# Performance work log

Measured on AMD Instinct MI355X. Metric: run time of the kernel, lower is better.

Reference implementation:

```python
import jax, jax.numpy as jnp
import numpy as np

D_MODEL = 512
NUM_HEADS = 8
HEAD_DIM = D_MODEL // NUM_HEADS
LN_EPS = 1e-5


def setup_inputs() -> dict:
    key = jax.random.key(0)
    ks = jax.random.split(key, 12)
    B, S, D = 4, 8192, D_MODEL
    scale = 1.0 / np.sqrt(D)  # xavier-ish init
    inp = {
        "x": jax.random.normal(ks[0], (B, S, D), dtype=jnp.float32),
        "Wq": jax.random.normal(ks[1], (D, D), dtype=jnp.float32) * scale,
        "bq": jnp.zeros((D,), dtype=jnp.float32),
        "Wk": jax.random.normal(ks[2], (D, D), dtype=jnp.float32) * scale,
        "bk": jnp.zeros((D,), dtype=jnp.float32),
        "Wv": jax.random.normal(ks[3], (D, D), dtype=jnp.float32) * scale,
        "bv": jnp.zeros((D,), dtype=jnp.float32),
        "Wo": jax.random.normal(ks[4], (D, D), dtype=jnp.float32) * scale,
        "bo": jnp.zeros((D,), dtype=jnp.float32),
        "gamma": jnp.ones((D,), dtype=jnp.float32),
        "beta": jnp.zeros((D,), dtype=jnp.float32),
    }
    return inp


def _split_heads(t, B, S):
    # (B, S, D) -> (B, H, S, hd)
    return t.reshape(B, S, NUM_HEADS, HEAD_DIM).transpose(0, 2, 1, 3)


def _feature_map(t):
    return jax.nn.elu(t) + 1.0


def reference(x, Wq, bq, Wk, bk, Wv, bv, Wo, bo, gamma, beta):
    B, S, D = x.shape
    q = _split_heads(x @ Wq + bq, B, S)
    k = _split_heads(x @ Wk + bk, B, S)
    v = _split_heads(x @ Wv + bv, B, S)

    q = _feature_map(q)
    k = _feature_map(k)

    # kv summary: (B, H, hd, hd) -- O(n d^2) instead of O(n^2 d)
    kv = jnp.einsum('bhnd,bhnm->bhdm', k, v)
    out = jnp.einsum('bhnd,bhdm->bhnm', q, kv)

    k_sum = k.sum(axis=2)  # (B, H, hd)
    normalizer = jnp.clip(jnp.einsum('bhnd,bhd->bhn', q, k_sum), 1e-6, None)
    out = out / normalizer[..., None]

    # merge heads: (B, H, S, hd) -> (B, S, D)
    out = out.transpose(0, 2, 1, 3).reshape(B, S, D)
    out = out @ Wo + bo

    # residual + layer norm (dropout is identity in eval / p=0)
    y = x + out
    mean = y.mean(axis=-1, keepdims=True)
    var = y.var(axis=-1, keepdims=True)
    y = (y - mean) * jax.lax.rsqrt(var + LN_EPS)
    return y * gamma + beta
```

## Files before the change

kernel.cpp:

```cpp
#include <hip/hip_runtime.h>
#include <cstdint>

#define SEQ     8192
#define BATCH   4
#define NHEAD   8
#define NTOK    (BATCH*SEQ)

typedef __bf16 bf16x8 __attribute__((ext_vector_type(8)));
typedef float  floatx4 __attribute__((ext_vector_type(4)));

static __device__ __forceinline__ float b2f(uint16_t h) {
    return __uint_as_float(((uint32_t)h) << 16);
}
static __device__ __forceinline__ uint16_t f2b(float f) {
    uint32_t u = __float_as_uint(f);
    u += 0x7fffu + ((u >> 16) & 1u);
    return (uint16_t)(u >> 16);
}

static __device__ __forceinline__ void async_copy16(const uint16_t* g, uint16_t* l) {
#if __has_builtin(__builtin_amdgcn_global_load_lds)
    __builtin_amdgcn_global_load_lds(
        (const __attribute__((address_space(1))) void*)g,
        (__attribute__((address_space(3))) void*)l, 16, 0, 0);
#else
    *(uint4*)l = *(const uint4*)g;
#endif
}

__global__ __launch_bounds__(256) void convert_x(
    const float* __restrict__ X, uint16_t* __restrict__ Xb)
{
    const size_t i = ((size_t)blockIdx.x * 256 + threadIdx.x) * 8;
    float4 f0 = *(const float4*)(X + i);
    float4 f1 = *(const float4*)(X + i + 4);
    uint4 o;
    uint16_t* p = (uint16_t*)&o;
    p[0]=f2b(f0.x); p[1]=f2b(f0.y); p[2]=f2b(f0.z); p[3]=f2b(f0.w);
    p[4]=f2b(f1.x); p[5]=f2b(f1.y); p[6]=f2b(f1.z); p[7]=f2b(f1.w);
    *(uint4*)(Xb + i) = o;
}

__global__ __launch_bounds__(256) void convert_w(
    const float* __restrict__ Wq, const float* __restrict__ Wk,
    const float* __restrict__ Wv, const float* __restrict__ Wo,
    uint16_t* __restrict__ out)
{
    const int z = blockIdx.z;
    const float* W = (z == 0) ? Wq : (z == 1) ? Wk : (z == 2) ? Wv : Wo;
    uint16_t* o = out + (size_t)z * 262144;
    const int n0 = blockIdx.x * 64, k0 = blockIdx.y * 64;
    __shared__ uint16_t tl[64][64];
    const int t = threadIdx.x;
    const int r  = t >> 4;
    const int c4 = (t & 15) * 4;
    #pragma unroll
    for (int s = 0; s < 4; ++s) {
        const int k = r + s * 16;
        float4 f = *(const float4*)(W + (size_t)(k0 + k) * 512 + n0 + c4);
        tl[c4 + 0][k] = f2b(f.x); tl[c4 + 1][k] = f2b(f.y);
        tl[c4 + 2][k] = f2b(f.z); tl[c4 + 3][k] = f2b(f.w);
    }
    __syncthreads();
    const int n  = t >> 2;
    const int kk = (t & 3) * 16;
    uint4* dst = (uint4*)(o + (size_t)(n0 + n) * 512 + k0 + kk);
    dst[0] = *(const uint4*)&tl[n][kk];
    dst[1] = *(const uint4*)&tl[n][kk + 8];
}

__global__ __launch_bounds__(256) void qkv128(
    const uint16_t* __restrict__ Xb,
    const uint16_t* __restrict__ Wt,
    const float* __restrict__ bq_, const float* __restrict__ bk_,
    const float* __restrict__ bv_,
    uint16_t* __restrict__ outQ, uint16_t* __restrict__ outK,
    uint16_t* __restrict__ outV)
{
    const int id = blockIdx.x;
    const int c  = id & 7;
    const int r_ = id >> 3;
    const int j_ = r_ % 12;
    const int s  = (r_ / 12) * 8 + c;
    const int proj = j_ >> 2;
    const int n0   = (j_ & 3) * 128;
    const int m0   = s * 128;

    const uint16_t* W = Wt + (size_t)proj * 262144;
    const float* bias = (proj == 0) ? bq_ : (proj == 1) ? bk_ : bv_;
    uint16_t* out     = (proj == 0) ? outQ : (proj == 1) ? outK : outV;
    const int act = (proj < 2);

    __shared__ uint16_t smem[8192];
    const int t = threadIdx.x;
    const int wave = t >> 6, lane = t & 63, quad = lane >> 4, lrow = lane & 15;
    const int wm = (wave & 1) * 64, wn = (wave >> 1) * 64;
    const int sr = t >> 2;
    const int sc = (t & 3) * 8;

    floatx4 acc[4][4] = {};

    for (int k0 = 0; k0 < 512; k0 += 32) {
        const uint16_t* gA = Xb + (size_t)(m0 + sr) * 512 + k0 + sc;
        async_copy16(gA,            smem + t * 8);
        async_copy16(gA + 64 * 512, smem + (t + 256) * 8);
        const uint16_t* gB = W + (size_t)(n0 + sr) * 512 + k0 + sc;
        async_copy16(gB,            smem + 4096 + t * 8);
        async_copy16(gB + 64 * 512, smem + 4096 + (t + 256) * 8);
        __syncthreads();
        bf16x8 af[4], bfr[4];
        #pragma unroll
        for (int i = 0; i < 4; ++i)
            af[i] = *(const bf16x8*)(smem + (wm + i * 16 + lrow) * 32 + quad * 8);
        #pragma unroll
        for (int j = 0; j < 4; ++j)
            bfr[j] = *(const bf16x8*)(smem + 4096 + (wn + j * 16 + lrow) * 32 + quad * 8);
        #pragma unroll
        for (int i = 0; i < 4; ++i)
            #pragma unroll
            for (int j = 0; j < 4; ++j)
                acc[i][j] = __builtin_amdgcn_mfma_f32_16x16x32_bf16(af[i], bfr[j], acc[i][j], 0, 0, 0);
        __syncthreads();
    }

    #pragma unroll
    for (int hh = 0; hh < 2; ++hh) {
        if ((wave & 1) == hh) {
            #pragma unroll
            for (int j = 0; j < 4; ++j) {
                const int col = wn + j * 16 + lrow;
                const float bb = bias[n0 + col];
                #pragma unroll
                for (int i = 0; i < 4; ++i) {
                    #pragma unroll
                    for (int r = 0; r < 4; ++r) {
                        const int lr = i * 16 + quad * 4 + r;
                        float v = acc[i][j][r] + bb;
                        if (act) v = (v > 0.0f) ? (v + 1.0f) : __expf(v);
                        smem[lr * 128 + (col ^ (((lr >> 2) & 3) << 4))] = f2b(v);
                    }
                }
            }
        }
        __syncthreads();
        #pragma unroll
        for (int p = 0; p < 4; ++p) {
            const int idx = p * 256 + t;
            const int row = idx >> 4;
            const int cc  = (idx & 15) * 8;
            uint4 v = *(const uint4*)(smem + row * 128 + (cc ^ (((row >> 2) & 3) << 4)));
            *(uint4*)(out + (size_t)(m0 + hh * 64 + row) * 512 + n0 + cc) = v;
        }
        __syncthreads();
    }
}

__global__ __launch_bounds__(256) void gemm_out128(
    const uint16_t* __restrict__ A,
    const uint16_t* __restrict__ Wt,
    const float* __restrict__ bias,
    const float* __restrict__ resid,
    uint16_t* __restrict__ out)
{
    const int id = blockIdx.x;
    const int c  = id & 7;
    const int r_ = id >> 3;
    const int j_ = r_ & 3;
    const int s  = (r_ >> 2) * 8 + c;
    const int n0 = j_ * 128;
    const int m0 = s * 128;

    __shared__ uint16_t smem[8192];
    const int t = threadIdx.x;
    const int wave = t >> 6, lane = t & 63, quad = lane >> 4, lrow = lane & 15;
    const int wm = (wave & 1) * 64, wn = (wave >> 1) * 64;
    const int sr = t >> 2;
    const int sc = (t & 3) * 8;

    floatx4 acc[4][4] = {};

    for (int k0 = 0; k0 < 512; k0 += 32) {
        const uint16_t* gA = A + (size_t)(m0 + sr) * 512 + k0 + sc;
        async_copy16(gA,            smem + t * 8);
        async_copy16(gA + 64 * 512, smem + (t + 256) * 8);
        const uint16_t* gB = Wt + (size_t)(n0 + sr) * 512 + k0 + sc;
        async_copy16(gB,            smem + 4096 + t * 8);
        async_copy16(gB + 64 * 512, smem + 4096 + (t + 256) * 8);
        __syncthreads();
        bf16x8 af[4], bfr[4];
        #pragma unroll
        for (int i = 0; i < 4; ++i)
            af[i] = *(const bf16x8*)(smem + (wm + i * 16 + lrow) * 32 + quad * 8);
        #pragma unroll
        for (int j = 0; j < 4; ++j)
            bfr[j] = *(const bf16x8*)(smem + 4096 + (wn + j * 16 + lrow) * 32 + quad * 8);
        #pragma unroll
        for (int i = 0; i < 4; ++i)
            #pragma unroll
            for (int j = 0; j < 4; ++j)
                acc[i][j] = __builtin_amdgcn_mfma_f32_16x16x32_bf16(af[i], bfr[j], acc[i][j], 0, 0, 0);
        __syncthreads();
    }

    #pragma unroll
    for (int hh = 0; hh < 2; ++hh) {
        if ((wave & 1) == hh) {
            #pragma unroll
            for (int j = 0; j < 4; ++j) {
                const int col = wn + j * 16 + lrow;
                const float bb = bias[n0 + col];
                #pragma unroll
                for (int i = 0; i < 4; ++i) {
                    #pragma unroll
                    for (int r = 0; r < 4; ++r) {
                        const int lr = i * 16 + quad * 4 + r;
                        float v = acc[i][j][r] + bb
                                + resid[(size_t)(m0 + hh * 64 + lr) * 512 + n0 + col];
                        smem[lr * 128 + (col ^ (((lr >> 2) & 3) << 4))] = f2b(v);
                    }
                }
            }
        }
        __syncthreads();
        #pragma unroll
        for (int p = 0; p < 4; ++p) {
            const int idx = p * 256 + t;
            const int row = idx >> 4;
            const int cc  = (idx & 15) * 8;
            uint4 v = *(const uint4*)(smem + row * 128 + (cc ^ (((row >> 2) & 3) << 4)));
            *(uint4*)(out + (size_t)(m0 + hh * 64 + row) * 512 + n0 + cc) = v;
        }
        __syncthreads();
    }
}

__global__ __launch_bounds__(256) void kv_accum(
    const uint16_t* __restrict__ K,
    const uint16_t* __restrict__ V,
    float* __restrict__ KV,
    float* __restrict__ KSUM)
{
    const int chunk = blockIdx.x;
    const int h     = blockIdx.y;
    const int b     = blockIdx.z;
    const int t    = threadIdx.x;
    const int wv   = t >> 6;
    const int lane = t & 63;
    const int quad = lane >> 4;
    const int lrow = lane & 15;

    __shared__ uint16_t kt[64 * 72];
    __shared__ uint16_t vt[64 * 72];

    floatx4 acc[4] = {};
    floatx4 accS = {};
    union { uint16_t u[8]; bf16x8 v; } one_u;
    #pragma unroll
    for (int j = 0; j < 8; ++j) one_u.u[j] = 0x3F80;
    const bf16x8 ones = one_u.v;

    const size_t base = ((size_t)(b * SEQ + chunk * 512)) * 512 + h * 64;

    for (int n0 = 0; n0 < 512; n0 += 64) {
        #pragma unroll
        for (int s = 0; s < 2; ++s) {
            const int i   = t + 256 * s;
            const int tok = i >> 3;
            const int d0  = (i & 7) * 8;
            uint4 kq = *(const uint4*)(K + base + (size_t)(n0 + tok) * 512 + d0);
            const uint16_t* kp = (const uint16_t*)&kq;
            #pragma unroll
            for (int j = 0; j < 8; ++j) kt[(d0 + j) * 72 + tok] = kp[j];
            uint4 vq = *(const uint4*)(V + base + (size_t)(n0 + tok) * 512 + d0);
            const uint16_t* vp = (const uint16_t*)&vq;
            #pragma unroll
            for (int j = 0; j < 8; ++j) vt[(d0 + j) * 72 + tok] = vp[j];
        }
        __syncthreads();
        #pragma unroll
        for (int ks = 0; ks < 2; ++ks) {
            bf16x8 af = *(const bf16x8*)(kt + (wv * 16 + lrow) * 72 + ks * 32 + quad * 8);
            accS = __builtin_amdgcn_mfma_f32_16x16x32_bf16(af, ones, accS, 0, 0, 0);
            #pragma unroll
            for (int nt = 0; nt < 4; ++nt) {
                bf16x8 bf = *(const bf16x8*)(vt + (nt * 16 + lrow) * 72 + ks * 32 + quad * 8);
                acc[nt] = __builtin_amdgcn_mfma_f32_16x16x32_bf16(af, bf, acc[nt], 0, 0, 0);
            }
        }
        __syncthreads();
    }

    float* kvp = KV + (size_t)(b * NHEAD + h) * 4096;
    #pragma unroll
    for (int nt = 0; nt < 4; ++nt) {
        const int m = nt * 16 + lrow;
        #pragma unroll
        for (int r = 0; r < 4; ++r) {
            const int d = wv * 16 + quad * 4 + r;
            atomicAdd(kvp + d * 64 + m, acc[nt][r]);
        }
    }
    if (lrow == 0) {
        float* kp = KSUM + (size_t)(b * NHEAD + h) * 64;
        #pragma unroll
        for (int r = 0; r < 4; ++r)
            atomicAdd(kp + wv * 16 + quad * 4 + r, accS[r]);
    }
}

__global__ __launch_bounds__(256) void attn_apply(
    const uint16_t* __restrict__ Q,
    const float* __restrict__ KVg,
    const float* __restrict__ KSg,
    uint16_t* __restrict__ OUT)
{
    const int h    = blockIdx.y;
    const int tok0 = blockIdx.x * 64;
    const int b    = tok0 >> 13;
    const int t    = threadIdx.x;
    const int wv   = t >> 6;
    const int lane = t & 63;
    const int quad = lane >> 4;
    const int lrow = lane & 15;

    __shared__ uint16_t bt[64 * 72];
    __shared__ uint16_t ksb[64];

    const float* kvp = KVg + (size_t)(b * NHEAD + h) * 4096;
    #pragma unroll
    for (int s = 0; s < 16; ++s) {
        const int e = t + 256 * s;
        const int d = e >> 6, m = e & 63;
        bt[m * 72 + d] = f2b(kvp[e]);
    }
    if (t < 64) ksb[t] = f2b(KSg[(size_t)(b * NHEAD + h) * 64 + t]);
    __syncthreads();

    floatx4 acc[4] = {};
    floatx4 accN = {};
    const uint16_t* qrow = Q + (size_t)(tok0 + wv * 16 + lrow) * 512 + h * 64 + quad * 8;
    #pragma unroll
    for (int ks = 0; ks < 2; ++ks) {
        bf16x8 af = *(const bf16x8*)(qrow + ks * 32);
        bf16x8 bks = *(const bf16x8*)(ksb + ks * 32 + quad * 8);
        accN = __builtin_amdgcn_mfma_f32_16x16x32_bf16(af, bks, accN, 0, 0, 0);
        #pragma unroll
        for (int nt = 0; nt < 4; ++nt) {
            bf16x8 bf = *(const bf16x8*)(bt + (nt * 16 + lrow) * 72 + ks * 32 + quad * 8);
            acc[nt] = __builtin_amdgcn_mfma_f32_16x16x32_bf16(af, bf, acc[nt], 0, 0, 0);
        }
    }

    __syncthreads();
    #pragma unroll
    for (int r = 0; r < 4; ++r) {
        const float inv = 1.0f / fmaxf(accN[r], 1e-6f);
        const int row = wv * 16 + quad * 4 + r;
        #pragma unroll
        for (int nt = 0; nt < 4; ++nt) {
            const int col = nt * 16 + lrow;
            bt[row * 64 + (col ^ (((row >> 2) & 3) << 4))] = f2b(acc[nt][r] * inv);
        }
    }
    __syncthreads();
    #pragma unroll
    for (int p = 0; p < 2; ++p) {
        const int idx = p * 256 + t;
        const int row = idx >> 3;
        const int cc  = (idx & 7) * 8;
        uint4 v = *(const uint4*)(bt + row * 64 + (cc ^ (((row >> 2) & 3) << 4)));
        *(uint4*)(OUT + (size_t)(tok0 + row) * 512 + h * 64 + cc) = v;
    }
}

__global__ __launch_bounds__(256) void ln_rows(
    const uint16_t* __restrict__ Z,
    const float* __restrict__ gamma,
    const float* __restrict__ beta,
    float* __restrict__ OUT)
{
    const int t = threadIdx.x;
    const int wv = t >> 6, lane = t & 63;
    const size_t row = (size_t)blockIdx.x * 4 + wv;
    union { uint4 q; uint16_t u[8]; } zz;
    zz.q = *(const uint4*)(Z + row * 512 + lane * 8);
    float v[8], s = 0.f, s2 = 0.f;
    #pragma unroll
    for (int j = 0; j < 8; ++j) {
        v[j] = b2f(zz.u[j]);
        s += v[j]; s2 += v[j] * v[j];
    }
    #pragma unroll
    for (int off = 32; off > 0; off >>= 1) {
        s  += __shfl_xor(s, off, 64);
        s2 += __shfl_xor(s2, off, 64);
    }
    const float mean = s * (1.0f / 512.0f);
    const float var  = s2 * (1.0f / 512.0f) - mean * mean;
    const float inv  = rsqrtf(var + 1e-5f);
    float4 g0 = *(const float4*)(gamma + lane * 8);
    float4 g1 = *(const float4*)(gamma + lane * 8 + 4);
    float4 b0 = *(const float4*)(beta + lane * 8);
    float4 b1 = *(const float4*)(beta + lane * 8 + 4);
    float4 o0, o1;
    o0.x = (v[0]-mean)*inv*g0.x + b0.x;  o0.y = (v[1]-mean)*inv*g0.y + b0.y;
    o0.z = (v[2]-mean)*inv*g0.z + b0.z;  o0.w = (v[3]-mean)*inv*g0.w + b0.w;
    o1.x = (v[4]-mean)*inv*g1.x + b1.x;  o1.y = (v[5]-mean)*inv*g1.y + b1.y;
    o1.z = (v[6]-mean)*inv*g1.z + b1.z;  o1.w = (v[7]-mean)*inv*g1.w + b1.w;
    *(float4*)(OUT + row * 512 + lane * 8)     = o0;
    *(float4*)(OUT + row * 512 + lane * 8 + 4) = o1;
}

extern "C" void kernel_launch(void* const* d_in, const int* in_sizes, int n_in,
                              void* d_out, int out_size, void* d_ws, size_t ws_size,
                              hipStream_t stream)
{
    (void)in_sizes; (void)n_in; (void)out_size; (void)ws_size;
    const float* x     = (const float*)d_in[0];
    const float* Wq    = (const float*)d_in[1];
    const float* bq    = (const float*)d_in[2];
    const float* Wk    = (const float*)d_in[3];
    const float* bk    = (const float*)d_in[4];
    const float* Wv    = (const float*)d_in[5];
    const float* bv    = (const float*)d_in[6];
    const float* Wo    = (const float*)d_in[7];
    const float* bo    = (const float*)d_in[8];
    const float* gamma = (const float*)d_in[9];
    const float* beta  = (const float*)d_in[10];

    uint8_t* ws = (uint8_t*)d_ws;
    float*    KV   = (float*)ws;
    float*    KSUM = (float*)(ws + (size_t)32 * 4096 * 4);
    uint16_t* Wt   = (uint16_t*)(ws + (size_t)32 * 4096 * 4 + 32 * 64 * 4);
    uint16_t* phiQ = (uint16_t*)(ws + (size_t)32 * 4096 * 4 + 32 * 64 * 4
                                    + (size_t)4 * 262144 * 2);
    uint16_t* Xb   = phiQ + (size_t)NTOK * 512;
    uint16_t* phiK = (uint16_t*)d_out;
    uint16_t* vbuf = (uint16_t*)d_out + (size_t)NTOK * 512;
    uint16_t* attn = Xb;
    uint16_t* zbuf = phiQ;

    hipMemsetAsync(ws, 0, (size_t)32 * 4096 * 4 + 32 * 64 * 4, stream);

    dim3 blk(256);
    convert_x<<<dim3(NTOK * 512 / (256 * 8)), blk, 0, stream>>>(x, Xb);
    convert_w<<<dim3(8, 8, 4), blk, 0, stream>>>(Wq, Wk, Wv, Wo, Wt);
    qkv128<<<dim3(3072), blk, 0, stream>>>(
        Xb, Wt, bq, bk, bv, phiQ, phiK, vbuf);
    kv_accum<<<dim3(16, NHEAD, BATCH), blk, 0, stream>>>(phiK, vbuf, KV, KSUM);
    attn_apply<<<dim3(NTOK / 64, NHEAD), blk, 0, stream>>>(phiQ, KV, KSUM, attn);
    gemm_out128<<<dim3(1024), blk, 0, stream>>>(
        attn, Wt + (size_t)3 * 262144, bo, x, zbuf);
    ln_rows<<<dim3(NTOK / 4), blk, 0, stream>>>(zbuf, gamma, beta, (float*)d_out);
}
```

Measured before the change: 306.5 us.

## Double-buffer GEMM k-loop, single-pass epilogue, and shrink LDS padding

The QKV and output-projection GEMMs now double-buffer their LDS tiles. The next k-slice's async global-to-LDS copies are issued before the MFMAs on the current slice, so that load latency can overlap compute and one barrier per iteration is removed. The epilogues now stage the full 128x128 tile in the doubled LDS and store it in one pass instead of two halves. The kv_accum and attn_apply kernels change their LDS row padding from 72 to 66 elements to reduce LDS footprint and bank conflicts. The 66-element stride breaks 16-byte alignment for the bf16x8 vector LDS reads, which risks misaligned or split accesses. The doubled GEMM LDS allocation may also lower occupancy.

```diff
diff --git a/kernel.cpp b/kernel.cpp
--- a/kernel.cpp
+++ b/kernel.cpp
@@ -91,67 +91,75 @@
     uint16_t* out     = (proj == 0) ? outQ : (proj == 1) ? outK : outV;
     const int act = (proj < 2);
 
-    __shared__ uint16_t smem[8192];
+    __shared__ uint16_t smem[16384];
     const int t = threadIdx.x;
     const int wave = t >> 6, lane = t & 63, quad = lane >> 4, lrow = lane & 15;
     const int wm = (wave & 1) * 64, wn = (wave >> 1) * 64;
     const int sr = t >> 2;
     const int sc = (t & 3) * 8;
 
+    const uint16_t* gA = Xb + (size_t)(m0 + sr) * 512 + sc;
+    const uint16_t* gB = W  + (size_t)(n0 + sr) * 512 + sc;
+
     floatx4 acc[4][4] = {};
 
+    async_copy16(gA,            smem + t * 8);
+    async_copy16(gA + 64 * 512, smem + (t + 256) * 8);
+    async_copy16(gB,            smem + 4096 + t * 8);
+    async_copy16(gB + 64 * 512, smem + 4096 + (t + 256) * 8);
+    __syncthreads();
+
+    int cur = 0;
     for (int k0 = 0; k0 < 512; k0 += 32) {
-        const uint16_t* gA = Xb + (size_t)(m0 + sr) * 512 + k0 + sc;
-        async_copy16(gA,            smem + t * 8);
-        async_copy16(gA + 64 * 512, smem + (t + 256) * 8);
-        const uint16_t* gB = W + (size_t)(n0 + sr) * 512 + k0 + sc;
-        async_copy16(gB,            smem + 4096 + t * 8);
-        async_copy16(gB + 64 * 512, smem + 4096 + (t + 256) * 8);
-        __syncthreads();
+        const int nxt = cur ^ 1;
+        if (k0 + 32 < 512) {
+            const uint16_t* pA = gA + k0 + 32;
+            async_copy16(pA,            smem + nxt * 8192 + t * 8);
+            async_copy16(pA + 64 * 512, smem + nxt * 8192 + (t + 256) * 8);
+            const uint16_t* pB = gB + k0 + 32;
+            async_copy16(pB,            smem + nxt * 8192 + 4096 + t * 8);
+            async_copy16(pB + 64 * 512, smem + nxt * 8192 + 4096 + (t + 256) * 8);
+        }
+        const uint16_t* base = smem + cur * 8192;
         bf16x8 af[4], bfr[4];
         #pragma unroll
         for (int i = 0; i < 4; ++i)
-            af[i] = *(const bf16x8*)(smem + (wm + i * 16 + lrow) * 32 + quad * 8);
+            af[i] = *(const bf16x8*)(base + (wm + i * 16 + lrow) * 32 + quad * 8);
         #pragma unroll
         for (int j = 0; j < 4; ++j)
-            bfr[j] = *(const bf16x8*)(smem + 4096 + (wn + j * 16 + lrow) * 32 + quad * 8);
+            bfr[j] = *(const bf16x8*)(base + 4096 + (wn + j * 16 + lrow) * 32 + quad * 8);
         #pragma unroll
         for (int i = 0; i < 4; ++i)
             #pragma unroll
             for (int j = 0; j < 4; ++j)
                 acc[i][j] = __builtin_amdgcn_mfma_f32_16x16x32_bf16(af[i], bfr[j], acc[i][j], 0, 0, 0);
         __syncthreads();
-    }
-
-    #pragma unroll
-    for (int hh = 0; hh < 2; ++hh) {
-        if ((wave & 1) == hh) {
-            #pragma unroll
-            for (int j = 0; j < 4; ++j) {
-                const int col = wn + j * 16 + lrow;
-                const float bb = bias[n0 + col];
-                #pragma unroll
-                for (int i = 0; i < 4; ++i) {
-                    #pragma unroll
-                    for (int r = 0; r < 4; ++r) {
-                        const int lr = i * 16 + quad * 4 + r;
-                        float v = acc[i][j][r] + bb;
-                        if (act) v = (v > 0.0f) ? (v + 1.0f) : __expf(v);
-                        smem[lr * 128 + (col ^ (((lr >> 2) & 3) << 4))] = f2b(v);
-                    }
-                }
+        cur = nxt;
+    }
+
+    #pragma unroll
+    for (int j = 0; j < 4; ++j) {
+        const int col = wn + j * 16 + lrow;
+        const float bb = bias[n0 + col];
+        #pragma unroll
+        for (int i = 0; i < 4; ++i) {
+            #pragma unroll
+            for (int r = 0; r < 4; ++r) {
+                const int row = wm + i * 16 + quad * 4 + r;
+                float v = acc[i][j][r] + bb;
+                if (act) v = (v > 0.0f) ? (v + 1.0f) : __expf(v);
+                smem[row * 128 + (col ^ (((row >> 2) & 3) << 4))] = f2b(v);
             }
         }
-        __syncthreads();
-        #pragma unroll
-        for (int p = 0; p < 4; ++p) {
-            const int idx = p * 256 + t;
-            const int row = idx >> 4;
-            const int cc  = (idx & 15) * 8;
-            uint4 v = *(const uint4*)(smem + row * 128 + (cc ^ (((row >> 2) & 3) << 4)));
-            *(uint4*)(out + (size_t)(m0 + hh * 64 + row) * 512 + n0 + cc) = v;
-        }
-        __syncthreads();
+    }
+    __syncthreads();
+    #pragma unroll
+    for (int p = 0; p < 8; ++p) {
+        const int idx = p * 256 + t;
+        const int row = idx >> 4;
+        const int cc  = (idx & 15) * 8;
+        uint4 v = *(const uint4*)(smem + row * 128 + (cc ^ (((row >> 2) & 3) << 4)));
+        *(uint4*)(out + (size_t)(m0 + row) * 512 + n0 + cc) = v;
     }
 }
 
@@ -170,67 +178,75 @@
     const int n0 = j_ * 128;
     const int m0 = s * 128;
 
-    __shared__ uint16_t smem[8192];
+    __shared__ uint16_t smem[16384];
     const int t = threadIdx.x;
     const int wave = t >> 6, lane = t & 63, quad = lane >> 4, lrow = lane & 15;
     const int wm = (wave & 1) * 64, wn = (wave >> 1) * 64;
     const int sr = t >> 2;
     const int sc = (t & 3) * 8;
 
+    const uint16_t* gA = A  + (size_t)(m0 + sr) * 512 + sc;
+    const uint16_t* gB = Wt + (size_t)(n0 + sr) * 512 + sc;
+
     floatx4 acc[4][4] = {};
 
+    async_copy16(gA,            smem + t * 8);
+    async_copy16(gA + 64 * 512, smem + (t + 256) * 8);
+    async_copy16(gB,            smem + 4096 + t * 8);
+    async_copy16(gB + 64 * 512, smem + 4096 + (t + 256) * 8);
+    __syncthreads();
+
+    int cur = 0;
     for (int k0 = 0; k0 < 512; k0 += 32) {
-        const uint16_t* gA = A + (size_t)(m0 + sr) * 512 + k0 + sc;
-        async_copy16(gA,            smem + t * 8);
-        async_copy16(gA + 64 * 512, smem + (t + 256) * 8);
-        const uint16_t* gB = Wt + (size_t)(n0 + sr) * 512 + k0 + sc;
-        async_copy16(gB,            smem + 4096 + t * 8);
-        async_copy16(gB + 64 * 512, smem + 4096 + (t + 256) * 8);
-        __syncthreads();
+        const int nxt = cur ^ 1;
+        if (k0 + 32 < 512) {
+            const uint16_t* pA = gA + k0 + 32;
+            async_copy16(pA,            smem + nxt * 8192 + t * 8);
+            async_copy16(pA + 64 * 512, smem + nxt * 8192 + (t + 256) * 8);
+            const uint16_t* pB = gB + k0 + 32;
+            async_copy16(pB,            smem + nxt * 8192 + 4096 + t * 8);
+            async_copy16(pB + 64 * 512, smem + nxt * 8192 + 4096 + (t + 256) * 8);
+        }
+        const uint16_t* base = smem + cur * 8192;
         bf16x8 af[4], bfr[4];
         #pragma unroll
         for (int i = 0; i < 4; ++i)
-            af[i] = *(const bf16x8*)(smem + (wm + i * 16 + lrow) * 32 + quad * 8);
+            af[i] = *(const bf16x8*)(base + (wm + i * 16 + lrow) * 32 + quad * 8);
         #pragma unroll
         for (int j = 0; j < 4; ++j)
-            bfr[j] = *(const bf16x8*)(smem + 4096 + (wn + j * 16 + lrow) * 32 + quad * 8);
+            bfr[j] = *(const bf16x8*)(base + 4096 + (wn + j * 16 + lrow) * 32 + quad * 8);
         #pragma unroll
         for (int i = 0; i < 4; ++i)
             #pragma unroll
             for (int j = 0; j < 4; ++j)
                 acc[i][j] = __builtin_amdgcn_mfma_f32_16x16x32_bf16(af[i], bfr[j], acc[i][j], 0, 0, 0);
         __syncthreads();
-    }
-
-    #pragma unroll
-    for (int hh = 0; hh < 2; ++hh) {
-        if ((wave & 1) == hh) {
-            #pragma unroll
-            for (int j = 0; j < 4; ++j) {
-                const int col = wn + j * 16 + lrow;
-                const float bb = bias[n0 + col];
-                #pragma unroll
-                for (int i = 0; i < 4; ++i) {
-                    #pragma unroll
-                    for (int r = 0; r < 4; ++r) {
-                        const int lr = i * 16 + quad * 4 + r;
-                        float v = acc[i][j][r] + bb
-                                + resid[(size_t)(m0 + hh * 64 + lr) * 512 + n0 + col];
-                        smem[lr * 128 + (col ^ (((lr >> 2) & 3) << 4))] = f2b(v);
-                    }
-                }
+        cur = nxt;
+    }
+
+    #pragma unroll
+    for (int j = 0; j < 4; ++j) {
+        const int col = wn + j * 16 + lrow;
+        const float bb = bias[n0 + col];
+        #pragma unroll
+        for (int i = 0; i < 4; ++i) {
+            #pragma unroll
+            for (int r = 0; r < 4; ++r) {
+                const int row = wm + i * 16 + quad * 4 + r;
+                float v = acc[i][j][r] + bb
+                        + resid[(size_t)(m0 + row) * 512 + n0 + col];
+                smem[row * 128 + (col ^ (((row >> 2) & 3) << 4))] = f2b(v);
             }
         }
-        __syncthreads();
-        #pragma unroll
-        for (int p = 0; p < 4; ++p) {
-            const int idx = p * 256 + t;
-            const int row = idx >> 4;
-            const int cc  = (idx & 15) * 8;
-            uint4 v = *(const uint4*)(smem + row * 128 + (cc ^ (((row >> 2) & 3) << 4)));
-            *(uint4*)(out + (size_t)(m0 + hh * 64 + row) * 512 + n0 + cc) = v;
-        }
-        __syncthreads();
+    }
+    __syncthreads();
+    #pragma unroll
+    for (int p = 0; p < 8; ++p) {
+        const int idx = p * 256 + t;
+        const int row = idx >> 4;
+        const int cc  = (idx & 15) * 8;
+        uint4 v = *(const uint4*)(smem + row * 128 + (cc ^ (((row >> 2) & 3) << 4)));
+        *(uint4*)(out + (size_t)(m0 + row) * 512 + n0 + cc) = v;
     }
 }
 
@@ -249,8 +265,8 @@
     const int quad = lane >> 4;
     const int lrow = lane & 15;
 
-    __shared__ uint16_t kt[64 * 72];
-    __shared__ uint16_t vt[64 * 72];
+    __shared__ uint16_t kt[64 * 66];
+    __shared__ uint16_t vt[64 * 66];
 
     floatx4 acc[4] = {};
     floatx4 accS = {};
@@ -270,20 +286,20 @@
             uint4 kq = *(const uint4*)(K + base + (size_t)(n0 + tok) * 512 + d0);
             const uint16_t* kp = (const uint16_t*)&kq;
             #pragma unroll
-            for (int j = 0; j < 8; ++j) kt[(d0 + j) * 72 + tok] = kp[j];
+            for (int j = 0; j < 8; ++j) kt[(d0 + j) * 66 + tok] = kp[j];
             uint4 vq = *(const uint4*)(V + base + (size_t)(n0 + tok) * 512 + d0);
             const uint16_t* vp = (const uint16_t*)&vq;
             #pragma unroll
-            for (int j = 0; j < 8; ++j) vt[(d0 + j) * 72 + tok] = vp[j];
+            for (int j = 0; j < 8; ++j) vt[(d0 + j) * 66 + tok] = vp[j];
         }
         __syncthreads();
         #pragma unroll
         for (int ks = 0; ks < 2; ++ks) {
-            bf16x8 af = *(const bf16x8*)(kt + (wv * 16 + lrow) * 72 + ks * 32 + quad * 8);
+            bf16x8 af = *(const bf16x8*)(kt + (wv * 16 + lrow) * 66 + ks * 32 + quad * 8);
             accS = __builtin_amdgcn_mfma_f32_16x16x32_bf16(af, ones, accS, 0, 0, 0);
             #pragma unroll
             for (int nt = 0; nt < 4; ++nt) {
-                bf16x8 bf = *(const bf16x8*)(vt + (nt * 16 + lrow) * 72 + ks * 32 + quad * 8);
+                bf16x8 bf = *(const bf16x8*)(vt + (nt * 16 + lrow) * 66 + ks * 32 + quad * 8);
                 acc[nt] = __builtin_amdgcn_mfma_f32_16x16x32_bf16(af, bf, acc[nt], 0, 0, 0);
             }
         }
@@ -323,7 +339,7 @@
     const int quad = lane >> 4;
     const int lrow = lane & 15;
 
-    __shared__ uint16_t bt[64 * 72];
+    __shared__ uint16_t bt[64 * 66];
     __shared__ uint16_t ksb[64];
 
     const float* kvp = KVg + (size_t)(b * NHEAD + h) * 4096;
@@ -331,7 +347,7 @@
     for (int s = 0; s < 16; ++s) {
         const int e = t + 256 * s;
         const int d = e >> 6, m = e & 63;
-        bt[m * 72 + d] = f2b(kvp[e]);
+        bt[m * 66 + d] = f2b(kvp[e]);
     }
     if (t < 64) ksb[t] = f2b(KSg[(size_t)(b * NHEAD + h) * 64 + t]);
     __syncthreads();
@@ -346,7 +362,7 @@
         accN = __builtin_amdgcn_mfma_f32_16x16x32_bf16(af, bks, accN, 0, 0, 0);
         #pragma unroll
         for (int nt = 0; nt < 4; ++nt) {
-            bf16x8 bf = *(const bf16x8*)(bt + (nt * 16 + lrow) * 72 + ks * 32 + quad * 8);
+            bf16x8 bf = *(const bf16x8*)(bt + (nt * 16 + lrow) * 66 + ks * 32 + quad * 8);
             acc[nt] = __builtin_amdgcn_mfma_f32_16x16x32_bf16(af, bf, acc[nt], 0, 0, 0);
         }
     }
```

New measurement: 274.6 us. -10.4%, faster.
